# Performance work log

Measured on AMD Instinct MI355X. Metric: run time of the kernel, lower is better.

Reference implementation:

```python
import jax, jax.numpy as jnp
import numpy as np
from jax import lax


def setup_inputs() -> dict:
    key = jax.random.key(0)
    kx, kw = jax.random.split(key)
    x = jax.random.normal(kx, (8, 32, 16, 160, 160), dtype=jnp.float32)
    # xavier-normal-ish init (scale irrelevant to correctness testing)
    weights = jax.random.normal(kw, (32, 32, 1, 3, 3), dtype=jnp.float32) * 0.1
    return {"x": x, "weights": weights}


def reference(x, weights):
    # per-(out_ch, in_ch) scale: mean |w| over kernel dims (2,3,4), detached
    scale = lax.stop_gradient(jnp.mean(jnp.abs(weights), axis=(2, 3, 4), keepdims=True))
    binary_no_grad = scale * jnp.sign(weights)          # {+-scale}
    clipped = jnp.clip(weights, -1.0, 1.0)
    # straight-through estimator: value = binary_no_grad, grad flows via clipped
    binary_weights = lax.stop_gradient(binary_no_grad - clipped) + clipped
    out = lax.conv_general_dilated(
        x, binary_weights,
        window_strides=(1, 1, 1),
        padding=((0, 0), (1, 1), (1, 1)),
        rhs_dilation=(1, 1, 1),
        dimension_numbers=("NCDHW", "OIDHW", "NCDHW"),
        feature_group_count=1,
    )
    return out
```

## Files before the change

kernel.cpp:

```cpp
#include <hip/hip_runtime.h>


typedef _Float16 half8 __attribute__((ext_vector_type(8)));
typedef float    floatx4 __attribute__((ext_vector_type(4)));

#define DHW  409600
#define HW   25600

__device__ __forceinline__ int lds_half_idx(int r, int w1, int kg) {
    const int w1x = w1 ^ ((w1 >> 2) & 1);
    const int skg = kg ^ (((w1 >> 1) ^ (w1 >> 3)) & 3);
    return (r * 162 + w1x) * 32 + skg * 8;
}

__global__ void bnn_wprep_kernel(const float* __restrict__ w,
                                 _Float16* __restrict__ ws) {
    const int tid = threadIdx.x;
    #pragma unroll
    for (int p4 = 0; p4 < 4; ++p4) {
        const int oi = tid * 4 + p4;
        const int o  = oi >> 5;
        const int i  = oi & 31;
        const float* wp = w + oi * 9;
        float s = 0.f;
        #pragma unroll
        for (int t = 0; t < 9; ++t) s += fabsf(wp[t]);
        s *= (1.f / 9.f);
        const int l = ((i >> 3) << 4) | (o & 15);
        const int p = o >> 4;
        const int j = i & 7;
        #pragma unroll
        for (int t = 0; t < 9; ++t) {
            const float v  = wp[t];
            const float sg = (v > 0.f) ? 1.f : ((v < 0.f) ? -1.f : 0.f);
            ws[((t * 2 + p) * 64 + l) * 8 + j] = (_Float16)(s * sg);
        }
    }
}

__global__ __launch_bounds__(512, 4) void bnn_conv3d_kernel(
        const float* __restrict__ x, const _Float16* __restrict__ ws,
        float* __restrict__ out) {
    __shared__ __align__(16) _Float16 ldsh[31104];

    const int tid  = threadIdx.x;
    const int lane = tid & 63;
    const int wid  = tid >> 6;

    const int bid = blockIdx.x;
    const int ht  = bid % 40;
    const int nd  = bid / 40;
    const int d   = nd & 15;
    const int n   = nd >> 4;
    const int h0  = ht * 4;

    const int  wq0 = tid % 40;
    const int  rs0 = tid / 40;
    const int  kg0 = rs0 & 3;
    const int  r0  = rs0 >> 2;
    const int  hi0 = h0 - 1 + r0;
    const bool v0l = (unsigned)hi0 < 160u;

    const bool act1 = tid < 448;
    const int  id1  = tid + 512;
    const int  wq1 = id1 % 40;
    const int  rs1 = id1 / 40;
    const int  kg1 = rs1 & 3;
    const int  r1  = rs1 >> 2;
    const int  hi1 = h0 - 1 + r1;
    const bool v1l = act1 && ((unsigned)hi1 < 160u);

    floatx4 fl0[8], fl1[8];
    {
        const floatx4 z = {0.f, 0.f, 0.f, 0.f};
        const float* s0 = x + ((n * 32 + kg0 * 8) * 16 + d) * HW + hi0 * 160 + wq0 * 4;
        const float* s1 = x + ((n * 32 + kg1 * 8) * 16 + d) * HW + hi1 * 160 + wq1 * 4;
        #pragma unroll
        for (int c = 0; c < 8; ++c)
            fl0[c] = v0l ? *reinterpret_cast<const floatx4*>(s0 + c * DHW) : z;
        #pragma unroll
        for (int c = 0; c < 8; ++c)
            fl1[c] = v1l ? *reinterpret_cast<const floatx4*>(s1 + c * DHW) : z;
    }

    if (tid < 192) {
        const int pos = tid >> 4, word = tid & 15;
        const int r   = pos >> 1;
        const int w1  = (pos & 1) ? 161 : 0;
        reinterpret_cast<unsigned int*>(ldsh)[(r * 162 + w1) * 16 + word] = 0u;
    }

    __builtin_amdgcn_sched_barrier(0);

    #pragma unroll
    for (int u = 0; u < 4; ++u) {
        half8 pk;
        #pragma unroll
        for (int c = 0; c < 8; ++c) pk[c] = (_Float16)fl0[c][u];
        const int w1 = wq0 * 4 + 1 + u;
        *reinterpret_cast<half8*>(&ldsh[lds_half_idx(r0, w1, kg0)]) = pk;
    }
    if (act1) {
        #pragma unroll
        for (int u = 0; u < 4; ++u) {
            half8 pk;
            #pragma unroll
            for (int c = 0; c < 8; ++c) pk[c] = (_Float16)fl1[c][u];
            const int w1 = wq1 * 4 + 1 + u;
            *reinterpret_cast<half8*>(&ldsh[lds_half_idx(r1, w1, kg1)]) = pk;
        }
    }

    half8 wf[2][9];
    {
        const half8* fb = reinterpret_cast<const half8*>(ws);
        #pragma unroll
        for (int t = 0; t < 9; ++t) {
            wf[0][t] = fb[(t * 2 + 0) * 64 + lane];
            wf[1][t] = fb[(t * 2 + 1) * 64 + lane];
        }
    }
    __syncthreads();

    const int s16   = lane & 15;
    const int kg    = lane >> 4;
    const int row   = wid & 3;
    const int whalf = wid >> 2;
    const int h     = h0 + row;
    const int obase = (n * 32 + s16) * DHW + d * HW + h * 160 + kg * 4;

    #pragma unroll
    for (int wtl = 0; wtl < 5; ++wtl) {
        const int wbase = (whalf * 5 + wtl) * 16;
        floatx4 acc0 = {0.f, 0.f, 0.f, 0.f};
        floatx4 acc1 = {0.f, 0.f, 0.f, 0.f};
        #pragma unroll
        for (int kw = 0; kw < 3; ++kw) {
            const int w1  = wbase + s16 + kw;
            const int w1x = w1 ^ ((w1 >> 2) & 1);
            const int sub = ((kg ^ (((w1 >> 1) ^ (w1 >> 3)) & 3)) * 8) + w1x * 32;
            #pragma unroll
            for (int kh = 0; kh < 3; ++kh) {
                const half8 a = *reinterpret_cast<const half8*>(
                        &ldsh[(row + kh) * (162 * 32) + sub]);
                const int t = kh * 3 + kw;
                acc0 = __builtin_amdgcn_mfma_f32_16x16x32_f16(a, wf[0][t], acc0, 0, 0, 0);
                acc1 = __builtin_amdgcn_mfma_f32_16x16x32_f16(a, wf[1][t], acc1, 0, 0, 0);
            }
        }
        float* op = out + obase + wbase;
        *reinterpret_cast<floatx4*>(op)            = acc0;
        *reinterpret_cast<floatx4*>(op + 16 * DHW) = acc1;
    }
}

extern "C" void kernel_launch(void* const* d_in, const int* in_sizes, int n_in,
                              void* d_out, int out_size, void* d_ws, size_t ws_size,
                              hipStream_t stream) {
    const float* x = (const float*)d_in[0];
    const float* w = (const float*)d_in[1];
    float* out = (float*)d_out;
    _Float16* ws = (_Float16*)d_ws;
    bnn_wprep_kernel<<<dim3(1), dim3(256), 0, stream>>>(w, ws);
    bnn_conv3d_kernel<<<dim3(5120), dim3(512), 0, stream>>>(x, ws, out);
}
```

Baseline: 206.0 us.

## Replace per-block halo tiles with a 6-row LDS ring and pipelined loads

Each block now covers 20 output rows instead of 4. Input rows stream through a 6-slot LDS ring buffer, and two register stages overlap global loads of upcoming rows with MFMA compute on the current ones. This removes the repeated halo-row loads (6 input rows per 4 output rows before) and the single load-then-compute phase. In exchange the grid shrinks to 1024 blocks of 320 threads, which reduces parallelism and may lower occupancy and latency hiding. It also adds four barriers per iteration pair.

```diff
diff --git a/kernel.cpp b/kernel.cpp
--- a/kernel.cpp
+++ b/kernel.cpp
@@ -6,11 +6,19 @@
 
 #define DHW  409600
 #define HW   25600
+#define ROWB (162*32)
 
-__device__ __forceinline__ int lds_half_idx(int r, int w1, int kg) {
+__device__ __forceinline__ int lds_half_idx(int slot, int w1, int kg) {
     const int w1x = w1 ^ ((w1 >> 2) & 1);
     const int skg = kg ^ (((w1 >> 1) ^ (w1 >> 3)) & 3);
-    return (r * 162 + w1x) * 32 + skg * 8;
+    return slot * ROWB + w1x * 32 + skg * 8;
+}
+
+__device__ __forceinline__ void barrier_raw() {
+    __builtin_amdgcn_sched_barrier(0);
+    asm volatile("s_waitcnt lgkmcnt(0)" ::: "memory");
+    __builtin_amdgcn_s_barrier();
+    __builtin_amdgcn_sched_barrier(0);
 }
 
 __global__ void bnn_wprep_kernel(const float* __restrict__ w,
@@ -38,119 +46,121 @@
     }
 }
 
-__global__ __launch_bounds__(512, 4) void bnn_conv3d_kernel(
+struct SR { floatx4 v[8]; };
+
+__global__ __launch_bounds__(320) void bnn_conv3d_ring(
         const float* __restrict__ x, const _Float16* __restrict__ ws,
         float* __restrict__ out) {
-    __shared__ __align__(16) _Float16 ldsh[31104];
+    __shared__ __align__(16) _Float16 ldsh[6 * ROWB];
 
     const int tid  = threadIdx.x;
     const int lane = tid & 63;
-    const int wid  = tid >> 6;
 
     const int bid = blockIdx.x;
-    const int ht  = bid % 40;
-    const int nd  = bid / 40;
+    const int chk = bid & 7;
+    const int nd  = bid >> 3;
     const int d   = nd & 15;
     const int n   = nd >> 4;
-    const int h0  = ht * 4;
+    const int h0  = chk * 20;
 
-    const int  wq0 = tid % 40;
-    const int  rs0 = tid / 40;
-    const int  kg0 = rs0 & 3;
-    const int  r0  = rs0 >> 2;
-    const int  hi0 = h0 - 1 + r0;
-    const bool v0l = (unsigned)hi0 < 160u;
+    const int wq   = tid % 40;
+    const int kg_s = (tid / 40) & 3;
+    const int rr   = tid / 160;
+    const float* xcol = x + ((n * 32 + kg_s * 8) * 16 + d) * HW + wq * 4;
 
-    const bool act1 = tid < 448;
-    const int  id1  = tid + 512;
-    const int  wq1 = id1 % 40;
-    const int  rs1 = id1 / 40;
-    const int  kg1 = rs1 & 3;
-    const int  r1  = rs1 >> 2;
-    const int  hi1 = h0 - 1 + r1;
-    const bool v1l = act1 && ((unsigned)hi1 < 160u);
+    const int s16  = lane & 15;
+    const int kg_r = lane >> 4;
+    const int f    = tid >> 6;
+    int rdoff[2][3];
+    #pragma unroll
+    for (int wt = 0; wt < 2; ++wt)
+        #pragma unroll
+        for (int kw = 0; kw < 3; ++kw)
+            rdoff[wt][kw] = lds_half_idx(0, f * 32 + wt * 16 + s16 + kw, kg_r);
+    float* obase = out + (n * 32 + s16) * DHW + d * HW + kg_r * 4 + f * 32;
 
-    floatx4 fl0[8], fl1[8];
+    half8 wf0[9], wf1[9];
     {
+        const half8* fb = reinterpret_cast<const half8*>(ws);
+        #pragma unroll
+        for (int t = 0; t < 9; ++t) {
+            wf0[t] = fb[(t * 2 + 0) * 64 + lane];
+            wf1[t] = fb[(t * 2 + 1) * 64 + lane];
+        }
+    }
+
+    auto ISSUE = [&](int k, SR& R) {
+        const int h_in = h0 + 2 * k - 1 + rr;
         const floatx4 z = {0.f, 0.f, 0.f, 0.f};
-        const float* s0 = x + ((n * 32 + kg0 * 8) * 16 + d) * HW + hi0 * 160 + wq0 * 4;
-        const float* s1 = x + ((n * 32 + kg1 * 8) * 16 + d) * HW + hi1 * 160 + wq1 * 4;
+        const float* p = xcol + h_in * 160;
+        const bool ok = (unsigned)h_in < 160u;
         #pragma unroll
         for (int c = 0; c < 8; ++c)
-            fl0[c] = v0l ? *reinterpret_cast<const floatx4*>(s0 + c * DHW) : z;
-        #pragma unroll
-        for (int c = 0; c < 8; ++c)
-            fl1[c] = v1l ? *reinterpret_cast<const floatx4*>(s1 + c * DHW) : z;
-    }
-
-    if (tid < 192) {
-        const int pos = tid >> 4, word = tid & 15;
-        const int r   = pos >> 1;
-        const int w1  = (pos & 1) ? 161 : 0;
-        reinterpret_cast<unsigned int*>(ldsh)[(r * 162 + w1) * 16 + word] = 0u;
-    }
-
-    __builtin_amdgcn_sched_barrier(0);
-
-    #pragma unroll
-    for (int u = 0; u < 4; ++u) {
-        half8 pk;
-        #pragma unroll
-        for (int c = 0; c < 8; ++c) pk[c] = (_Float16)fl0[c][u];
-        const int w1 = wq0 * 4 + 1 + u;
-        *reinterpret_cast<half8*>(&ldsh[lds_half_idx(r0, w1, kg0)]) = pk;
-    }
-    if (act1) {
+            R.v[c] = ok ? *reinterpret_cast<const floatx4*>(p + c * DHW) : z;
+    };
+    auto PACK = [&](int k, SR& R) {
+        const int slot = (2 * k + rr) % 6;
         #pragma unroll
         for (int u = 0; u < 4; ++u) {
             half8 pk;
             #pragma unroll
-            for (int c = 0; c < 8; ++c) pk[c] = (_Float16)fl1[c][u];
-            const int w1 = wq1 * 4 + 1 + u;
-            *reinterpret_cast<half8*>(&ldsh[lds_half_idx(r1, w1, kg1)]) = pk;
+            for (int c = 0; c < 8; ++c) pk[c] = (_Float16)R.v[c][u];
+            *reinterpret_cast<half8*>(
+                &ldsh[lds_half_idx(slot, wq * 4 + 1 + u, kg_s)]) = pk;
         }
-    }
-
-    half8 wf[2][9];
-    {
-        const half8* fb = reinterpret_cast<const half8*>(ws);
+        if (wq == 0) {
+            half8 zz = {};
+            *reinterpret_cast<half8*>(&ldsh[lds_half_idx(slot, 0, kg_s)]) = zz;
+        }
+        if (wq == 39) {
+            half8 zz = {};
+            *reinterpret_cast<half8*>(&ldsh[lds_half_idx(slot, 161, kg_s)]) = zz;
+        }
+    };
+    auto COMPUTE = [&](int t) {
         #pragma unroll
-        for (int t = 0; t < 9; ++t) {
-            wf[0][t] = fb[(t * 2 + 0) * 64 + lane];
-            wf[1][t] = fb[(t * 2 + 1) * 64 + lane];
-        }
-    }
-    __syncthreads();
-
-    const int s16   = lane & 15;
-    const int kg    = lane >> 4;
-    const int row   = wid & 3;
-    const int whalf = wid >> 2;
-    const int h     = h0 + row;
-    const int obase = (n * 32 + s16) * DHW + d * HW + h * 160 + kg * 4;
-
-    #pragma unroll
-    for (int wtl = 0; wtl < 5; ++wtl) {
-        const int wbase = (whalf * 5 + wtl) * 16;
-        floatx4 acc0 = {0.f, 0.f, 0.f, 0.f};
-        floatx4 acc1 = {0.f, 0.f, 0.f, 0.f};
-        #pragma unroll
-        for (int kw = 0; kw < 3; ++kw) {
-            const int w1  = wbase + s16 + kw;
-            const int w1x = w1 ^ ((w1 >> 2) & 1);
-            const int sub = ((kg ^ (((w1 >> 1) ^ (w1 >> 3)) & 3)) * 8) + w1x * 32;
+        for (int row_l = 0; row_l < 2; ++row_l) {
             #pragma unroll
-            for (int kh = 0; kh < 3; ++kh) {
-                const half8 a = *reinterpret_cast<const half8*>(
-                        &ldsh[(row + kh) * (162 * 32) + sub]);
-                const int t = kh * 3 + kw;
-                acc0 = __builtin_amdgcn_mfma_f32_16x16x32_f16(a, wf[0][t], acc0, 0, 0, 0);
-                acc1 = __builtin_amdgcn_mfma_f32_16x16x32_f16(a, wf[1][t], acc1, 0, 0, 0);
+            for (int wt = 0; wt < 2; ++wt) {
+                floatx4 a0 = {0.f, 0.f, 0.f, 0.f};
+                floatx4 a1 = {0.f, 0.f, 0.f, 0.f};
+                #pragma unroll
+                for (int kh = 0; kh < 3; ++kh) {
+                    const int slot = (2 * t + row_l + kh) % 6;
+                    const int so   = slot * ROWB;
+                    #pragma unroll
+                    for (int kw = 0; kw < 3; ++kw) {
+                        const half8 a = *reinterpret_cast<const half8*>(
+                                &ldsh[so + rdoff[wt][kw]]);
+                        const int tap = kh * 3 + kw;
+                        a0 = __builtin_amdgcn_mfma_f32_16x16x32_f16(a, wf0[tap], a0, 0, 0, 0);
+                        a1 = __builtin_amdgcn_mfma_f32_16x16x32_f16(a, wf1[tap], a1, 0, 0, 0);
+                    }
+                }
+                float* op = obase + (h0 + 2 * t + row_l) * 160 + wt * 16;
+                *reinterpret_cast<floatx4*>(op)            = a0;
+                *reinterpret_cast<floatx4*>(op + 16 * DHW) = a1;
             }
         }
-        float* op = out + obase + wbase;
-        *reinterpret_cast<floatx4*>(op)            = acc0;
-        *reinterpret_cast<floatx4*>(op + 16 * DHW) = acc1;
+    };
+
+    SR A, B;
+    ISSUE(0, A);
+    ISSUE(1, B);
+    PACK(0, A);
+    ISSUE(2, A);
+    for (int tt = 0; tt < 5; ++tt) {
+        const int t0 = 2 * tt;
+        barrier_raw();
+        PACK(t0 + 1, B);
+        barrier_raw();
+        if (t0 + 3 <= 10) ISSUE(t0 + 3, B);
+        COMPUTE(t0);
+        barrier_raw();
+        PACK(t0 + 2, A);
+        barrier_raw();
+        if (t0 + 4 <= 10) ISSUE(t0 + 4, A);
+        COMPUTE(t0 + 1);
     }
 }
 
@@ -162,5 +172,5 @@
     float* out = (float*)d_out;
     _Float16* ws = (_Float16*)d_ws;
     bnn_wprep_kernel<<<dim3(1), dim3(256), 0, stream>>>(w, ws);
-    bnn_conv3d_kernel<<<dim3(5120), dim3(512), 0, stream>>>(x, ws, out);
+    bnn_conv3d_ring<<<dim3(1024), dim3(320), 0, stream>>>(x, ws, out);
 }
```

After: 204.1 us. No clear change (-0.9%).

## Shrink conv tile to two output rows with 320-thread blocks and swizzled block order

Applied to the files above, without the earlier changes.

Each block now computes 2 output rows with 5 waves instead of 4 rows with 8 waves, so it loads 4 input rows instead of 6. The LDS tile drops its padded halo columns, and out-of-range width taps are masked in registers. Block IDs are remapped across 8 groups, likely to spread work across XCDs and improve cache locality. It also uses a raw barrier that waits only on LDS counters. The cost is more halo re-reads per output row (2x vertical overlap) and extra select logic, traded for higher occupancy and less LDS per block.

```diff
diff --git a/kernel.cpp b/kernel.cpp
--- a/kernel.cpp
+++ b/kernel.cpp
@@ -7,10 +7,17 @@
 #define DHW  409600
 #define HW   25600
 
-__device__ __forceinline__ int lds_half_idx(int r, int w1, int kg) {
-    const int w1x = w1 ^ ((w1 >> 2) & 1);
-    const int skg = kg ^ (((w1 >> 1) ^ (w1 >> 3)) & 3);
-    return (r * 162 + w1x) * 32 + skg * 8;
+__device__ __forceinline__ int lds_half_idx(int r, int w, int kg) {
+    const int wx  = w ^ ((w >> 2) & 1);
+    const int skg = kg ^ (((w >> 1) ^ (w >> 3)) & 3);
+    return (r * 160 + wx) * 32 + skg * 8;
+}
+
+__device__ __forceinline__ void barrier_raw() {
+    __builtin_amdgcn_sched_barrier(0);
+    asm volatile("s_waitcnt lgkmcnt(0)" ::: "memory");
+    __builtin_amdgcn_s_barrier();
+    __builtin_amdgcn_sched_barrier(0);
 }
 
 __global__ void bnn_wprep_kernel(const float* __restrict__ w,
@@ -38,58 +45,43 @@
     }
 }
 
-__global__ __launch_bounds__(512, 4) void bnn_conv3d_kernel(
+__global__ __launch_bounds__(320, 5) void bnn_conv3d_kernel(
         const float* __restrict__ x, const _Float16* __restrict__ ws,
         float* __restrict__ out) {
-    __shared__ __align__(16) _Float16 ldsh[31104];
+    __shared__ __align__(16) _Float16 ldsh[4 * 160 * 32];
 
     const int tid  = threadIdx.x;
     const int lane = tid & 63;
     const int wid  = tid >> 6;
 
     const int bid = blockIdx.x;
-    const int ht  = bid % 40;
-    const int nd  = bid / 40;
+    const int wk  = (bid & 7) * 1280 + (bid >> 3);
+    const int ht  = wk % 80;
+    const int nd  = wk / 80;
     const int d   = nd & 15;
     const int n   = nd >> 4;
-    const int h0  = ht * 4;
+    const int h0  = ht * 2;
 
-    const int  wq0 = tid % 40;
-    const int  rs0 = tid / 40;
-    const int  kg0 = rs0 & 3;
-    const int  r0  = rs0 >> 2;
-    const int  hi0 = h0 - 1 + r0;
-    const bool v0l = (unsigned)hi0 < 160u;
+    const int wq0 = tid % 40, kg0 = (tid / 40) & 3, r0 = tid / 160;
+    const int id1 = tid + 320;
+    const int wq1 = id1 % 40, kg1 = (id1 / 40) & 3, r1 = id1 / 160;
+    const int hi0 = h0 - 1 + r0;
+    const int hi1 = h0 - 1 + r1;
 
-    const bool act1 = tid < 448;
-    const int  id1  = tid + 512;
-    const int  wq1 = id1 % 40;
-    const int  rs1 = id1 / 40;
-    const int  kg1 = rs1 & 3;
-    const int  r1  = rs1 >> 2;
-    const int  hi1 = h0 - 1 + r1;
-    const bool v1l = act1 && ((unsigned)hi1 < 160u);
-
+    const floatx4 z4 = {0.f, 0.f, 0.f, 0.f};
     floatx4 fl0[8], fl1[8];
     {
-        const floatx4 z = {0.f, 0.f, 0.f, 0.f};
         const float* s0 = x + ((n * 32 + kg0 * 8) * 16 + d) * HW + hi0 * 160 + wq0 * 4;
-        const float* s1 = x + ((n * 32 + kg1 * 8) * 16 + d) * HW + hi1 * 160 + wq1 * 4;
+        const bool ok0 = (unsigned)hi0 < 160u;
         #pragma unroll
         for (int c = 0; c < 8; ++c)
-            fl0[c] = v0l ? *reinterpret_cast<const floatx4*>(s0 + c * DHW) : z;
+            fl0[c] = ok0 ? *reinterpret_cast<const floatx4*>(s0 + c * DHW) : z4;
+        const float* s1 = x + ((n * 32 + kg1 * 8) * 16 + d) * HW + hi1 * 160 + wq1 * 4;
+        const bool ok1 = (unsigned)hi1 < 160u;
         #pragma unroll
         for (int c = 0; c < 8; ++c)
-            fl1[c] = v1l ? *reinterpret_cast<const floatx4*>(s1 + c * DHW) : z;
+            fl1[c] = ok1 ? *reinterpret_cast<const floatx4*>(s1 + c * DHW) : z4;
     }
-
-    if (tid < 192) {
-        const int pos = tid >> 4, word = tid & 15;
-        const int r   = pos >> 1;
-        const int w1  = (pos & 1) ? 161 : 0;
-        reinterpret_cast<unsigned int*>(ldsh)[(r * 162 + w1) * 16 + word] = 0u;
-    }
-
     __builtin_amdgcn_sched_barrier(0);
 
     #pragma unroll
@@ -97,60 +89,64 @@
         half8 pk;
         #pragma unroll
         for (int c = 0; c < 8; ++c) pk[c] = (_Float16)fl0[c][u];
-        const int w1 = wq0 * 4 + 1 + u;
-        *reinterpret_cast<half8*>(&ldsh[lds_half_idx(r0, w1, kg0)]) = pk;
+        *reinterpret_cast<half8*>(&ldsh[lds_half_idx(r0, wq0 * 4 + u, kg0)]) = pk;
     }
-    if (act1) {
+    #pragma unroll
+    for (int u = 0; u < 4; ++u) {
+        half8 pk;
         #pragma unroll
-        for (int u = 0; u < 4; ++u) {
-            half8 pk;
-            #pragma unroll
-            for (int c = 0; c < 8; ++c) pk[c] = (_Float16)fl1[c][u];
-            const int w1 = wq1 * 4 + 1 + u;
-            *reinterpret_cast<half8*>(&ldsh[lds_half_idx(r1, w1, kg1)]) = pk;
-        }
+        for (int c = 0; c < 8; ++c) pk[c] = (_Float16)fl1[c][u];
+        *reinterpret_cast<half8*>(&ldsh[lds_half_idx(r1, wq1 * 4 + u, kg1)]) = pk;
     }
+    __builtin_amdgcn_sched_barrier(0);
 
-    half8 wf[2][9];
+    half8 wf0[9], wf1[9];
     {
         const half8* fb = reinterpret_cast<const half8*>(ws);
         #pragma unroll
         for (int t = 0; t < 9; ++t) {
-            wf[0][t] = fb[(t * 2 + 0) * 64 + lane];
-            wf[1][t] = fb[(t * 2 + 1) * 64 + lane];
+            wf0[t] = fb[(t * 2 + 0) * 64 + lane];
+            wf1[t] = fb[(t * 2 + 1) * 64 + lane];
         }
     }
-    __syncthreads();
+    barrier_raw();
 
-    const int s16   = lane & 15;
-    const int kg    = lane >> 4;
-    const int row   = wid & 3;
-    const int whalf = wid >> 2;
-    const int h     = h0 + row;
-    const int obase = (n * 32 + s16) * DHW + d * HW + h * 160 + kg * 4;
+    const int s16  = lane & 15;
+    const int kg_r = lane >> 4;
+    const half8 zh = {};
+    float* ob = out + (n * 32 + s16) * DHW + d * HW + kg_r * 4;
 
     #pragma unroll
-    for (int wtl = 0; wtl < 5; ++wtl) {
-        const int wbase = (whalf * 5 + wtl) * 16;
-        floatx4 acc0 = {0.f, 0.f, 0.f, 0.f};
-        floatx4 acc1 = {0.f, 0.f, 0.f, 0.f};
+    for (int q = 0; q < 2; ++q) {
+        const int g = wid + q * 5;
         #pragma unroll
-        for (int kw = 0; kw < 3; ++kw) {
-            const int w1  = wbase + s16 + kw;
-            const int w1x = w1 ^ ((w1 >> 2) & 1);
-            const int sub = ((kg ^ (((w1 >> 1) ^ (w1 >> 3)) & 3)) * 8) + w1x * 32;
+        for (int rl = 0; rl < 2; ++rl) {
+            floatx4 a0 = z4, a1 = z4;
             #pragma unroll
             for (int kh = 0; kh < 3; ++kh) {
-                const half8 a = *reinterpret_cast<const half8*>(
-                        &ldsh[(row + kh) * (162 * 32) + sub]);
-                const int t = kh * 3 + kw;
-                acc0 = __builtin_amdgcn_mfma_f32_16x16x32_f16(a, wf[0][t], acc0, 0, 0, 0);
-                acc1 = __builtin_amdgcn_mfma_f32_16x16x32_f16(a, wf[1][t], acc1, 0, 0, 0);
+                #pragma unroll
+                for (int kw = 0; kw < 3; ++kw) {
+                    const int w_in = g * 16 + s16 + kw - 1;
+                    half8 a;
+                    if ((q == 0 && kw == 0) || (q == 1 && kw == 2)) {
+                        const bool ok = (unsigned)w_in < 160u;
+                        const int wrd = ok ? w_in : (w_in < 0 ? 0 : 159);
+                        a = *reinterpret_cast<const half8*>(
+                                &ldsh[lds_half_idx(rl + kh, wrd, kg_r)]);
+                        a = ok ? a : zh;
+                    } else {
+                        a = *reinterpret_cast<const half8*>(
+                                &ldsh[lds_half_idx(rl + kh, w_in, kg_r)]);
+                    }
+                    const int t = kh * 3 + kw;
+                    a0 = __builtin_amdgcn_mfma_f32_16x16x32_f16(a, wf0[t], a0, 0, 0, 0);
+                    a1 = __builtin_amdgcn_mfma_f32_16x16x32_f16(a, wf1[t], a1, 0, 0, 0);
+                }
             }
+            float* op = ob + (h0 + rl) * 160 + g * 16;
+            *reinterpret_cast<floatx4*>(op)            = a0;
+            *reinterpret_cast<floatx4*>(op + 16 * DHW) = a1;
         }
-        float* op = out + obase + wbase;
-        *reinterpret_cast<floatx4*>(op)            = acc0;
-        *reinterpret_cast<floatx4*>(op + 16 * DHW) = acc1;
     }
 }
 
@@ -162,5 +158,5 @@
     float* out = (float*)d_out;
     _Float16* ws = (_Float16*)d_ws;
     bnn_wprep_kernel<<<dim3(1), dim3(256), 0, stream>>>(w, ws);
-    bnn_conv3d_kernel<<<dim3(5120), dim3(512), 0, stream>>>(x, ws, out);
+    bnn_conv3d_kernel<<<dim3(10240), dim3(320), 0, stream>>>(x, ws, out);
 }
```

New measurement: 360.1 us. 1.75x slower.

## Process four depth slices per block with register-prefetched software pipeline

Applied to the files above, without the earlier changes.

Each block now handles four consecutive depth slices instead of one, cutting the grid to a quarter of the blocks. The next slice's global loads are issued into registers while the current slice is computed from LDS, which overlaps memory latency with MFMA work. Weight fragments are loaded once per block. Each wave now covers one output-channel half over all width tiles instead of both halves over half the width. Out-of-range rows are clamped and zeroed at pack time. The cost is fewer blocks in flight, which may leave the device less saturated at the tail, plus the extra barriers.

```diff
diff --git a/kernel.cpp b/kernel.cpp
--- a/kernel.cpp
+++ b/kernel.cpp
@@ -6,11 +6,19 @@
 
 #define DHW  409600
 #define HW   25600
+#define ROWB (162*32)
 
-__device__ __forceinline__ int lds_half_idx(int r, int w1, int kg) {
+__device__ __forceinline__ int swz(int w1, int kg) {
     const int w1x = w1 ^ ((w1 >> 2) & 1);
     const int skg = kg ^ (((w1 >> 1) ^ (w1 >> 3)) & 3);
-    return (r * 162 + w1x) * 32 + skg * 8;
+    return w1x * 32 + skg * 8;
+}
+
+__device__ __forceinline__ void barrier_raw() {
+    __builtin_amdgcn_sched_barrier(0);
+    asm volatile("s_waitcnt lgkmcnt(0)" ::: "memory");
+    __builtin_amdgcn_s_barrier();
+    __builtin_amdgcn_sched_barrier(0);
 }
 
 __global__ void bnn_wprep_kernel(const float* __restrict__ w,
@@ -38,50 +46,103 @@
     }
 }
 
-__global__ __launch_bounds__(512, 4) void bnn_conv3d_kernel(
+__global__ __launch_bounds__(512, 4) void bnn_conv3d_pipe(
         const float* __restrict__ x, const _Float16* __restrict__ ws,
         float* __restrict__ out) {
-    __shared__ __align__(16) _Float16 ldsh[31104];
+    __shared__ __align__(16) _Float16 ldsh[6 * ROWB];
 
     const int tid  = threadIdx.x;
     const int lane = tid & 63;
     const int wid  = tid >> 6;
 
     const int bid = blockIdx.x;
-    const int ht  = bid % 40;
-    const int nd  = bid / 40;
-    const int d   = nd & 15;
-    const int n   = nd >> 4;
+    const int dq  = bid & 3;
+    const int ht  = (bid >> 2) % 40;
+    const int n   = bid / 160;
     const int h0  = ht * 4;
+    const int d0  = dq * 4;
 
-    const int  wq0 = tid % 40;
-    const int  rs0 = tid / 40;
-    const int  kg0 = rs0 & 3;
-    const int  r0  = rs0 >> 2;
-    const int  hi0 = h0 - 1 + r0;
-    const bool v0l = (unsigned)hi0 < 160u;
+    const int  wq0 = tid % 40, kg0 = (tid / 40) & 3, r0 = tid / 160;
+    const int  id1 = tid + 512;
+    const int  wq1 = id1 % 40, kg1 = (id1 / 40) & 3, r1 = id1 / 160;
+    const bool act1 = tid < 448;
+    const int  hi0 = h0 - 1 + r0,  hi1 = h0 - 1 + r1;
+    const bool ok0 = (unsigned)hi0 < 160u, ok1 = (unsigned)hi1 < 160u;
+    const int  hc0 = ok0 ? hi0 : (hi0 < 0 ? 0 : 159);
+    const int  hc1 = ok1 ? hi1 : (hi1 < 0 ? 0 : 159);
+    const float* xb0 = x + (n * 32 + kg0 * 8) * DHW + hc0 * 160 + wq0 * 4;
+    const float* xb1 = x + (n * 32 + kg1 * 8) * DHW + hc1 * 160 + wq1 * 4;
 
-    const bool act1 = tid < 448;
-    const int  id1  = tid + 512;
-    const int  wq1 = id1 % 40;
-    const int  rs1 = id1 / 40;
-    const int  kg1 = rs1 & 3;
-    const int  r1  = rs1 >> 2;
-    const int  hi1 = h0 - 1 + r1;
-    const bool v1l = act1 && ((unsigned)hi1 < 160u);
+    const int s16  = lane & 15;
+    const int kg_r = lane >> 4;
+    const int row  = wid & 3;
+    const int oh   = wid >> 2;
 
-    floatx4 fl0[8], fl1[8];
-    {
-        const floatx4 z = {0.f, 0.f, 0.f, 0.f};
-        const float* s0 = x + ((n * 32 + kg0 * 8) * 16 + d) * HW + hi0 * 160 + wq0 * 4;
-        const float* s1 = x + ((n * 32 + kg1 * 8) * 16 + d) * HW + hi1 * 160 + wq1 * 4;
+    floatx4 A[8], B[8];
+
+    auto ISSUE = [&](int d, floatx4* R0, floatx4* R1) {
+        const float* p0 = xb0 + d * HW;
         #pragma unroll
         for (int c = 0; c < 8; ++c)
-            fl0[c] = v0l ? *reinterpret_cast<const floatx4*>(s0 + c * DHW) : z;
+            R0[c] = *reinterpret_cast<const floatx4*>(p0 + c * DHW);
+        if (act1) {
+            const float* p1 = xb1 + d * HW;
+            #pragma unroll
+            for (int c = 0; c < 8; ++c)
+                R1[c] = *reinterpret_cast<const floatx4*>(p1 + c * DHW);
+        }
+    };
+    auto PACK = [&](floatx4* R0, floatx4* R1) {
         #pragma unroll
-        for (int c = 0; c < 8; ++c)
-            fl1[c] = v1l ? *reinterpret_cast<const floatx4*>(s1 + c * DHW) : z;
-    }
+        for (int u = 0; u < 4; ++u) {
+            half8 pk;
+            #pragma unroll
+            for (int c = 0; c < 8; ++c)
+                pk[c] = ok0 ? (_Float16)R0[c][u] : (_Float16)0.f;
+            *reinterpret_cast<half8*>(
+                &ldsh[r0 * ROWB + swz(wq0 * 4 + 1 + u, kg0)]) = pk;
+        }
+        if (act1) {
+            #pragma unroll
+            for (int u = 0; u < 4; ++u) {
+                half8 pk;
+                #pragma unroll
+                for (int c = 0; c < 8; ++c)
+                    pk[c] = ok1 ? (_Float16)R1[c][u] : (_Float16)0.f;
+                *reinterpret_cast<half8*>(
+                    &ldsh[r1 * ROWB + swz(wq1 * 4 + 1 + u, kg1)]) = pk;
+            }
+        }
+    };
+
+    half8 wf[9];
+
+    auto COMPUTE = [&](int d) {
+        float* ob = out + (n * 32 + oh * 16 + s16) * DHW + d * HW
+                        + (h0 + row) * 160 + kg_r * 4;
+        #pragma unroll
+        for (int gp = 0; gp < 5; ++gp) {
+            const int ga = gp * 2, gb = gp * 2 + 1;
+            floatx4 aa = {0.f, 0.f, 0.f, 0.f};
+            floatx4 ab = {0.f, 0.f, 0.f, 0.f};
+            #pragma unroll
+            for (int kh = 0; kh < 3; ++kh) {
+                const int rb = (row + kh) * ROWB;
+                #pragma unroll
+                for (int kw = 0; kw < 3; ++kw) {
+                    const half8 fa = *reinterpret_cast<const half8*>(
+                            &ldsh[rb + swz(ga * 16 + s16 + kw, kg_r)]);
+                    const half8 fb = *reinterpret_cast<const half8*>(
+                            &ldsh[rb + swz(gb * 16 + s16 + kw, kg_r)]);
+                    const int t = kh * 3 + kw;
+                    aa = __builtin_amdgcn_mfma_f32_16x16x32_f16(fa, wf[t], aa, 0, 0, 0);
+                    ab = __builtin_amdgcn_mfma_f32_16x16x32_f16(fb, wf[t], ab, 0, 0, 0);
+                }
+            }
+            *reinterpret_cast<floatx4*>(ob + ga * 16) = aa;
+            *reinterpret_cast<floatx4*>(ob + gb * 16) = ab;
+        }
+    };
 
     if (tid < 192) {
         const int pos = tid >> 4, word = tid & 15;
@@ -90,68 +151,32 @@
         reinterpret_cast<unsigned int*>(ldsh)[(r * 162 + w1) * 16 + word] = 0u;
     }
 
+    ISSUE(d0 + 0, A, B);
+    {
+        const half8* fbp = reinterpret_cast<const half8*>(ws);
+        #pragma unroll
+        for (int t = 0; t < 9; ++t)
+            wf[t] = fbp[(t * 2 + oh) * 64 + lane];
+    }
     __builtin_amdgcn_sched_barrier(0);
-
-    #pragma unroll
-    for (int u = 0; u < 4; ++u) {
-        half8 pk;
-        #pragma unroll
-        for (int c = 0; c < 8; ++c) pk[c] = (_Float16)fl0[c][u];
-        const int w1 = wq0 * 4 + 1 + u;
-        *reinterpret_cast<half8*>(&ldsh[lds_half_idx(r0, w1, kg0)]) = pk;
-    }
-    if (act1) {
-        #pragma unroll
-        for (int u = 0; u < 4; ++u) {
-            half8 pk;
-            #pragma unroll
-            for (int c = 0; c < 8; ++c) pk[c] = (_Float16)fl1[c][u];
-            const int w1 = wq1 * 4 + 1 + u;
-            *reinterpret_cast<half8*>(&ldsh[lds_half_idx(r1, w1, kg1)]) = pk;
-        }
-    }
-
-    half8 wf[2][9];
-    {
-        const half8* fb = reinterpret_cast<const half8*>(ws);
-        #pragma unroll
-        for (int t = 0; t < 9; ++t) {
-            wf[0][t] = fb[(t * 2 + 0) * 64 + lane];
-            wf[1][t] = fb[(t * 2 + 1) * 64 + lane];
-        }
-    }
-    __syncthreads();
-
-    const int s16   = lane & 15;
-    const int kg    = lane >> 4;
-    const int row   = wid & 3;
-    const int whalf = wid >> 2;
-    const int h     = h0 + row;
-    const int obase = (n * 32 + s16) * DHW + d * HW + h * 160 + kg * 4;
-
-    #pragma unroll
-    for (int wtl = 0; wtl < 5; ++wtl) {
-        const int wbase = (whalf * 5 + wtl) * 16;
-        floatx4 acc0 = {0.f, 0.f, 0.f, 0.f};
-        floatx4 acc1 = {0.f, 0.f, 0.f, 0.f};
-        #pragma unroll
-        for (int kw = 0; kw < 3; ++kw) {
-            const int w1  = wbase + s16 + kw;
-            const int w1x = w1 ^ ((w1 >> 2) & 1);
-            const int sub = ((kg ^ (((w1 >> 1) ^ (w1 >> 3)) & 3)) * 8) + w1x * 32;
-            #pragma unroll
-            for (int kh = 0; kh < 3; ++kh) {
-                const half8 a = *reinterpret_cast<const half8*>(
-                        &ldsh[(row + kh) * (162 * 32) + sub]);
-                const int t = kh * 3 + kw;
-                acc0 = __builtin_amdgcn_mfma_f32_16x16x32_f16(a, wf[0][t], acc0, 0, 0, 0);
-                acc1 = __builtin_amdgcn_mfma_f32_16x16x32_f16(a, wf[1][t], acc1, 0, 0, 0);
-            }
-        }
-        float* op = out + obase + wbase;
-        *reinterpret_cast<floatx4*>(op)            = acc0;
-        *reinterpret_cast<floatx4*>(op + 16 * DHW) = acc1;
-    }
+    PACK(A, B);
+    ISSUE(d0 + 1, A, B);
+    barrier_raw();
+    COMPUTE(d0 + 0);
+    barrier_raw();
+    PACK(A, B);
+    ISSUE(d0 + 2, A, B);
+    barrier_raw();
+    COMPUTE(d0 + 1);
+    barrier_raw();
+    PACK(A, B);
+    ISSUE(d0 + 3, A, B);
+    barrier_raw();
+    COMPUTE(d0 + 2);
+    barrier_raw();
+    PACK(A, B);
+    barrier_raw();
+    COMPUTE(d0 + 3);
 }
 
 extern "C" void kernel_launch(void* const* d_in, const int* in_sizes, int n_in,
@@ -162,5 +187,5 @@
     float* out = (float*)d_out;
     _Float16* ws = (_Float16*)d_ws;
     bnn_wprep_kernel<<<dim3(1), dim3(256), 0, stream>>>(w, ws);
-    bnn_conv3d_kernel<<<dim3(5120), dim3(512), 0, stream>>>(x, ws, out);
+    bnn_conv3d_pipe<<<dim3(1280), dim3(512), 0, stream>>>(x, ws, out);
 }
```

After: 324.4 us. +57.5%, slower.
